# Kernel optimization log

Measured on AMD Instinct MI355X. Metric: run time of the kernel, lower is better.

Reference implementation:

```python
import jax, jax.numpy as jnp
import numpy as np

B = 4096
D_INPUT = 20
CTX = 10
IN_DIM = CTX * (D_INPUT + 1) + D_INPUT  # 230
D_MODEL = 256
N_LAYERS = 12
D_STATE = 16
D_CONV = 4
EXPAND = 2
D_INNER = EXPAND * D_MODEL  # 512
DT_RANK = (D_MODEL + 15) // 16  # ceil(256/16) = 16


def setup_inputs() -> dict:
    key = jax.random.key(0)
    ks = jax.random.split(key, 12)
    s = lambda k, shape, scale=0.02: jax.random.normal(k, shape, jnp.float32) * scale
    A = jnp.broadcast_to(jnp.arange(1, D_STATE + 1, dtype=jnp.float32), (N_LAYERS, D_INNER, D_STATE))
    return {
        "x": jax.random.normal(ks[0], (B, IN_DIM), jnp.float32),
        "Wi": s(ks[1], (IN_DIM, D_MODEL)),
        "bi": jnp.zeros((D_MODEL,), jnp.float32),
        "in_proj_w": s(ks[2], (N_LAYERS, D_MODEL, 2 * D_INNER)),
        "conv_w": s(ks[3], (N_LAYERS, D_INNER, D_CONV), 0.3),
        "conv_b": jnp.zeros((N_LAYERS, D_INNER), jnp.float32),
        "x_proj_w": s(ks[4], (N_LAYERS, D_INNER, DT_RANK + 2 * D_STATE)),
        "dt_proj_w": s(ks[5], (N_LAYERS, DT_RANK, D_INNER), 0.1),
        "dt_proj_b": jnp.full((N_LAYERS, D_INNER), -4.6, jnp.float32),  # softplus -> small dt
        "A_log": jnp.log(A),  # S4D-real init as in mamba_ssm
        "D": jnp.ones((N_LAYERS, D_INNER), jnp.float32),
        "out_proj_w": s(ks[6], (N_LAYERS, D_INNER, D_MODEL)),
        "Wo": s(ks[7], (D_MODEL, 1)),
        "bo": jnp.zeros((1,), jnp.float32),
    }


def _mamba_block(h, in_proj, conv_w, conv_b, x_proj, dt_w, dt_b, A_log, Dp, out_proj):
    # h: (B, L, D_MODEL)
    Bn, L, _ = h.shape
    xz = h @ in_proj                       # (B, L, 2*D_INNER)
    xr, z = jnp.split(xz, 2, axis=-1)
    # causal depthwise conv1d, kernel D_CONV, left-pad D_CONV-1
    xp = jnp.pad(xr, ((0, 0), (D_CONV - 1, 0), (0, 0)))
    win = jnp.stack([xp[:, k:k + L, :] for k in range(D_CONV)], axis=-1)  # (B,L,C,K)
    xc = jnp.einsum('blck,ck->blc', win, conv_w) + conv_b
    xc = jax.nn.silu(xc)
    dbl = xc @ x_proj                      # (B, L, DT_RANK + 2*D_STATE)
    dt, Bm, Cm = jnp.split(dbl, [DT_RANK, DT_RANK + D_STATE], axis=-1)
    dt = jax.nn.softplus(dt @ dt_w + dt_b)  # (B, L, D_INNER)
    A = -jnp.exp(A_log)                     # (D_INNER, D_STATE)
    dA = jnp.exp(dt[..., None] * A)                              # (B,L,di,ds)
    dBu = dt[..., None] * Bm[:, :, None, :] * xc[..., None]      # (B,L,di,ds)

    def step(hs, inp):
        dA_t, dBu_t, C_t = inp
        hs = dA_t * hs + dBu_t             # (B, di, ds)
        y_t = jnp.einsum('bds,bs->bd', hs, C_t)
        return hs, y_t

    h0 = jnp.zeros((Bn, D_INNER, D_STATE), h.dtype)
    _, ys = jax.lax.scan(step, h0, (dA.swapaxes(0, 1), dBu.swapaxes(0, 1), Cm.swapaxes(0, 1)))
    y = ys.swapaxes(0, 1)                  # (B, L, D_INNER)
    y = y + xc * Dp
    y = y * jax.nn.silu(z)
    return y @ out_proj                    # (B, L, D_MODEL)


def reference(x, Wi, bi, in_proj_w, conv_w, conv_b, x_proj_w, dt_proj_w, dt_proj_b, A_log, D, out_proj_w, Wo, bo):
    h = (x @ Wi + bi)[:, None, :]          # (B, 1, D_MODEL) -- unsqueeze(1)
    for i in range(N_LAYERS):
        h = _mamba_block(h, in_proj_w[i], conv_w[i], conv_b[i], x_proj_w[i],
                         dt_proj_w[i], dt_proj_b[i], A_log[i], D[i], out_proj_w[i])
    h = h[:, 0, :]                         # squeeze(1)
    return h @ Wo + bo                     # (B, 1)
```

## Files before the change

### kernel.cpp

```cpp
#include <hip/hip_runtime.h>
#include <hip/hip_fp8.h>
#include <math.h>

#define NB 4096
#define IN_D 230
#define DM 256
#define NL 12
#define DST 16
#define DI 512
#define DTR 16
#define XPN 48
#define XB 528
#define HB 272

typedef __attribute__((ext_vector_type(4))) float floatx4;
typedef __attribute__((ext_vector_type(2))) float floatx2;
typedef __attribute__((ext_vector_type(2))) long long2v;
typedef __attribute__((ext_vector_type(4))) int intx4;
typedef __attribute__((ext_vector_type(8))) int intx8;

__device__ __forceinline__ float silu_f(float x) {
    return x * __builtin_amdgcn_rcpf(1.0f + __expf(-x));
}
__device__ __forceinline__ float softplus_f(float x) {
    return (x > 20.0f) ? x : __logf(1.0f + __expf(x));
}

__device__ __forceinline__ unsigned char f2fp8(float x) {
#if __has_builtin(__builtin_amdgcn_cvt_pk_fp8_f32)
    return (unsigned char)(__builtin_amdgcn_cvt_pk_fp8_f32(x, x, 0, false) & 0xff);
#else
    __hip_fp8_e4m3 t(x); return (unsigned char)t.__x;
#endif
}
__device__ __forceinline__ float fp82f(unsigned char b) {
#if __has_builtin(__builtin_amdgcn_cvt_f32_fp8)
    return __builtin_amdgcn_cvt_f32_fp8((int)b, 0);
#else
    __hip_fp8_e4m3 t; t.__x = (__hip_fp8_storage_t)b; return (float)t;
#endif
}

__device__ __forceinline__ unsigned f2fp4(float x) {
    float ax = fabsf(x);
    unsigned s = (x < 0.0f) ? 8u : 0u;
    unsigned m;
    if      (ax < 0.25f) m = 0;
    else if (ax < 0.75f) m = 1;
    else if (ax < 1.25f) m = 2;
    else if (ax < 1.75f) m = 3;
    else if (ax < 2.50f) m = 4;
    else if (ax < 3.50f) m = 5;
    else if (ax < 5.00f) m = 6;
    else                 m = 7;
    return s | m;
}

__global__ __launch_bounds__(256) void pack_all(
    const float* __restrict__ x,
    const float* __restrict__ Wi, const float* __restrict__ ip,
    const float* __restrict__ op, const float* __restrict__ xp,
    const float* __restrict__ dtw,
    const float* __restrict__ cw, const float* __restrict__ cb,
    const float* __restrict__ db, const float* __restrict__ Dv,
    unsigned char* __restrict__ xpad,
    unsigned char* __restrict__ WiT, unsigned char* __restrict__ dtwP,
    unsigned char* __restrict__ ip4, unsigned char* __restrict__ op4,
    unsigned char* __restrict__ xp4,
    floatx2* __restrict__ cwcb, floatx2* __restrict__ dbdv)
{
    __shared__ float tbuf[64][65];
    const int fid = blockIdx.x;

    if (fid < 1264) {
        const float* src; unsigned char* dst;
        int K, N, ngK, t;
        bool isfp4;
        if (fid < 16) {
            src = Wi; dst = WiT; K = IN_D; N = DM; ngK = 4; t = fid; isfp4 = false;
        } else if (fid < 784) {
            int local = fid - 16; int l = local >> 6; t = local & 63;
            K = DM; N = 2 * DI; ngK = 4; isfp4 = true;
            src = ip + (size_t)l * K * N; dst = ip4 + (size_t)l * 131072;
        } else if (fid < 1168) {
            int local = fid - 784; int l = local >> 5; t = local & 31;
            K = DI; N = DM; ngK = 8; isfp4 = true;
            src = op + (size_t)l * K * N; dst = op4 + (size_t)l * 65536;
        } else {
            int local = fid - 1168; int l = local >> 3; t = local & 7;
            K = DI; N = XPN; ngK = 8; isfp4 = true;
            src = xp + (size_t)l * K * N; dst = xp4 + (size_t)l * 16384;
        }
        const int g = t % ngK, nb = t / ngK;
        const int k0 = g * 64, n0 = nb * 64;
        {
            const int r = threadIdx.x >> 6, c = threadIdx.x & 63;
#pragma unroll
            for (int i = 0; i < 16; i++) {
                int kk = k0 + i * 4 + r;
                int nn = n0 + c;
                tbuf[i * 4 + r][c] = (kk < K && nn < N) ? src[(size_t)kk * N + nn] : 0.0f;
            }
        }
        __syncthreads();
        if (!isfp4) {
            const int cbi = threadIdx.x >> 6;
            const int lane = threadIdx.x & 63;
            const int q = lane >> 4, m16 = lane & 15;
            const int chunk = (nb * 4 + cbi) * ngK + g;
            union { unsigned char b[16]; intx4 v; } buf;
#pragma unroll
            for (int sub = 0; sub < 2; sub++)
#pragma unroll
                for (int byt = 0; byt < 8; byt++) {
                    int k = sub * 32 + q * 8 + byt;
                    int n = cbi * 16 + m16;
                    buf.b[sub * 8 + byt] = f2fp8(tbuf[k][n]);
                }
            *(intx4*)(dst + (size_t)chunk * 1024 + lane * 16) = buf.v;
        } else {
            const int kg = g >> 1, half = g & 1;
            const int nkg128 = ngK >> 1;
            const int cbi = threadIdx.x >> 6;
            const int rem = threadIdx.x & 63;
            const int q4loc = rem >> 5;
            const int hb = (rem >> 4) & 1;
            const int m16 = rem & 15;
            const int q4 = half * 2 + q4loc;
            const int chunk = (nb * 4 + cbi) * nkg128 + kg;
            union { unsigned char b[8]; long v; } buf;
#pragma unroll
            for (int bl = 0; bl < 8; bl++) {
                unsigned ob = 0;
#pragma unroll
                for (int i = 0; i < 2; i++) {
                    int k_tile = q4loc * 32 + hb * 16 + bl * 2 + i;
                    float v = tbuf[k_tile][cbi * 16 + m16] * 128.0f;
                    ob |= f2fp4(v) << (i * 4);
                }
                buf.b[bl] = (unsigned char)ob;
            }
            *(long*)(dst + (size_t)chunk * 1024 + (q4 * 16 + m16) * 16 + hb * 8) = buf.v;
        }
    } else if (fid < 2032) {
        int local = fid - 1264;
        int l = local >> 6, bx = local & 63;
        int idx = bx * 256 + threadIdx.x;
        int chunk = idx >> 9;
        int rr = idx & 511;
        int lane = rr >> 3, byt = rr & 7;
        int q = lane >> 4, m16 = lane & 15;
        int col = chunk * 16 + m16;
        int k = q * 8 + byt;
        float v = (k < DTR) ? dtw[(size_t)l * DTR * DI + (size_t)k * DI + col] : 0.0f;
        dtwP[(size_t)l * 16384 + idx] = f2fp8(v);
    } else if (fid < 2056) {
        int idx = (fid - 2032) * 256 + threadIdx.x;
        floatx2 v; v.x = cw[(size_t)idx * 4 + 3]; v.y = cb[idx];
        cwcb[idx] = v;
    } else if (fid < 2080) {
        int idx = (fid - 2056) * 256 + threadIdx.x;
        floatx2 v; v.x = db[idx]; v.y = Dv[idx];
        dbdv[idx] = v;
    } else {
        int idx = (fid - 2080) * 256 + threadIdx.x;
        int r = idx >> 8, k = idx & 255;
        float v = (k < IN_D) ? x[(size_t)r * IN_D + k] : 0.0f;
        xpad[idx] = f2fp8(v);
    }
}

__global__ __launch_bounds__(1024) void mamba_all(
    const unsigned char* __restrict__ xpad, const unsigned char* __restrict__ WiT,
    const float* __restrict__ bi,
    const unsigned char* __restrict__ ip4, const unsigned char* __restrict__ op4,
    const unsigned char* __restrict__ xp4, const unsigned char* __restrict__ dtwP,
    const floatx2* __restrict__ cwcb, const floatx2* __restrict__ dbdv,
    const float* __restrict__ Wo, const float* __restrict__ bo,
    float* __restrict__ out)
{
    __shared__ unsigned char hs[16 * HB];
    __shared__ unsigned char xcs[16 * XB];
    __shared__ unsigned char szs[16 * XB];
    __shared__ float dbls[16 * 68];

    const int tid = threadIdx.x;
    const int w = tid >> 6, lane = tid & 63;
    const int q = lane >> 4, m16 = lane & 15;
    const int rb = blockIdx.x * 16;
    const long2v z2 = (long2v){0, 0};

    {
        floatx4 a0 = (floatx4){0.f, 0.f, 0.f, 0.f};
        floatx4 a1 = (floatx4){0.f, 0.f, 0.f, 0.f};
        const unsigned char* Ap = xpad + (size_t)(rb + m16) * DM + q * 8;
        const unsigned char* Bp = WiT + (size_t)(w * 4) * 1024 + lane * 16;
#pragma unroll
        for (int g = 0; g < 4; g++) {
            long2v b = *(const long2v*)(Bp + g * 1024);
            long av0 = *(const long*)(Ap + (g * 2) * 32);
            long av1 = *(const long*)(Ap + (g * 2 + 1) * 32);
            a0 = __builtin_amdgcn_mfma_f32_16x16x32_fp8_fp8(av0, b.x, a0, 0, 0, 0);
            a1 = __builtin_amdgcn_mfma_f32_16x16x32_fp8_fp8(av1, b.y, a1, 0, 0, 0);
        }
        a0 = a0 + a1;
        int col = w * 16 + m16;
#pragma unroll
        for (int r = 0; r < 4; r++)
            hs[(q * 4 + r) * HB + col] = f2fp8(a0[r] + bi[col]);
    }
    __syncthreads();

    for (int l = 0; l < NL; l++) {
        const unsigned char* ip = ip4 + (size_t)l * 131072;
        const unsigned char* xp = xp4 + (size_t)l * 16384;
        const unsigned char* op = op4 + (size_t)l * 65536;
        const unsigned char* dwp = dtwP + (size_t)l * 16384;
        const floatx2* cc = cwcb + (size_t)l * DI;
        const floatx2* dd = dbdv + (size_t)l * DI;

        {
            floatx4 acc[4];
#pragma unroll
            for (int t = 0; t < 4; t++) acc[t] = (floatx4){0.f, 0.f, 0.f, 0.f};
            const unsigned char* Bp = ip + (size_t)(w * 8) * 1024 + lane * 16;
            const unsigned char* Ar = hs + m16 * HB + q * 32;
#pragma unroll
            for (int kg = 0; kg < 2; kg++) {
                union { long2v h[2]; intx8 v; } av;
                av.h[0] = *(const long2v*)(Ar + kg * 128);
                av.h[1] = *(const long2v*)(Ar + kg * 128 + 16);
#pragma unroll
                for (int t = 0; t < 4; t++) {
                    union { long2v h[2]; intx8 v; } bv;
                    bv.h[0] = *(const long2v*)(Bp + (size_t)(t * 2 + kg) * 1024);
                    bv.h[1] = z2;
                    acc[t] = __builtin_amdgcn_mfma_scale_f32_16x16x128_f8f6f4(
                        av.v, bv.v, acc[t], 0, 4, 0, 127, 0, 120);
                }
            }
            if (w < 8) {
#pragma unroll
                for (int t = 0; t < 4; t++) {
                    int col = w * 64 + t * 16 + m16;
                    floatx2 c2 = cc[col];
#pragma unroll
                    for (int r = 0; r < 4; r++) {
                        float v = silu_f(acc[t][r] * c2.x + c2.y);
                        xcs[(q * 4 + r) * XB + col] = f2fp8(v);
                    }
                }
            } else {
#pragma unroll
                for (int t = 0; t < 4; t++)
#pragma unroll
                    for (int r = 0; r < 4; r++) {
                        int col = (w - 8) * 64 + t * 16 + m16;
                        szs[(q * 4 + r) * XB + col] = f2fp8(silu_f(acc[t][r]));
                    }
            }
        }
        __syncthreads();

        if (w < 4) {
            floatx4 acc = (floatx4){0.f, 0.f, 0.f, 0.f};
            const unsigned char* Bp = xp + (size_t)(w * 4) * 1024 + lane * 16;
            const unsigned char* Ar = xcs + m16 * XB + q * 32;
#pragma unroll
            for (int kg = 0; kg < 4; kg++) {
                union { long2v h[2]; intx8 v; } av;
                av.h[0] = *(const long2v*)(Ar + kg * 128);
                av.h[1] = *(const long2v*)(Ar + kg * 128 + 16);
                union { long2v h[2]; intx8 v; } bv;
                bv.h[0] = *(const long2v*)(Bp + (size_t)kg * 1024);
                bv.h[1] = z2;
                acc = __builtin_amdgcn_mfma_scale_f32_16x16x128_f8f6f4(
                    av.v, bv.v, acc, 0, 4, 0, 127, 0, 120);
            }
#pragma unroll
            for (int r = 0; r < 4; r++)
                dbls[(q * 4 + r) * 68 + w * 16 + m16] = acc[r];
        }
        __syncthreads();

        {
            const unsigned char* Wp = dwp + (size_t)(w * 2) * 512 + lane * 8;
            long b0 = *(const long*)(Wp);
            long b1 = *(const long*)(Wp + 512);
            const int c0 = w * 32 + m16, c1 = c0 + 16;
            const floatx2 dd0 = dd[c0], dd1 = dd[c1];

            const int brow = lane >> 2, bj = lane & 3;
            const float* dr0 = &dbls[brow * 68 + DTR];
            float p = dr0[bj]      * dr0[DST + bj]
                    + dr0[bj + 4]  * dr0[DST + bj + 4]
                    + dr0[bj + 8]  * dr0[DST + bj + 8]
                    + dr0[bj + 12] * dr0[DST + bj + 12];
            p += __shfl_xor(p, 1);
            p += __shfl_xor(p, 2);
            float bcr[4];
#pragma unroll
            for (int r = 0; r < 4; r++) bcr[r] = __shfl(p, (q * 4 + r) * 4);

            long afrag = 0;
            if (q < 2) {
                const float* dr = &dbls[m16 * 68 + q * 8];
                unsigned lo, hi;
                lo = __builtin_amdgcn_cvt_pk_fp8_f32(dr[0], dr[1], 0, false);
                lo = __builtin_amdgcn_cvt_pk_fp8_f32(dr[2], dr[3], lo, true);
                hi = __builtin_amdgcn_cvt_pk_fp8_f32(dr[4], dr[5], 0, false);
                hi = __builtin_amdgcn_cvt_pk_fp8_f32(dr[6], dr[7], hi, true);
                union { unsigned u[2]; long l; } av;
                av.u[0] = lo; av.u[1] = hi;
                afrag = av.l;
            }
            floatx4 d0v = (floatx4){dd0.x, dd0.x, dd0.x, dd0.x};
            floatx4 d1v = (floatx4){dd1.x, dd1.x, dd1.x, dd1.x};
            d0v = __builtin_amdgcn_mfma_f32_16x16x32_fp8_fp8(afrag, b0, d0v, 0, 0, 0);
            d1v = __builtin_amdgcn_mfma_f32_16x16x32_fp8_fp8(afrag, b1, d1v, 0, 0, 0);
#pragma unroll
            for (int r = 0; r < 4; r++) {
                int row = q * 4 + r;
                int off0 = row * XB + c0;
                float v0 = (softplus_f(d0v[r]) * bcr[r] + dd0.y) * fp82f(xcs[off0]) * fp82f(szs[off0]);
                xcs[off0] = f2fp8(v0);
                int off1 = off0 + 16;
                float v1 = (softplus_f(d1v[r]) * bcr[r] + dd1.y) * fp82f(xcs[off1]) * fp82f(szs[off1]);
                xcs[off1] = f2fp8(v1);
            }
        }
        __syncthreads();

        {
            floatx4 acc = (floatx4){0.f, 0.f, 0.f, 0.f};
            const unsigned char* Bp = op + (size_t)(w * 4) * 1024 + lane * 16;
            const unsigned char* Ar = xcs + m16 * XB + q * 32;
#pragma unroll
            for (int kg = 0; kg < 4; kg++) {
                union { long2v h[2]; intx8 v; } av;
                av.h[0] = *(const long2v*)(Ar + kg * 128);
                av.h[1] = *(const long2v*)(Ar + kg * 128 + 16);
                union { long2v h[2]; intx8 v; } bv;
                bv.h[0] = *(const long2v*)(Bp + (size_t)kg * 1024);
                bv.h[1] = z2;
                acc = __builtin_amdgcn_mfma_scale_f32_16x16x128_f8f6f4(
                    av.v, bv.v, acc, 0, 4, 0, 127, 0, 120);
            }
            int col = w * 16 + m16;
#pragma unroll
            for (int r = 0; r < 4; r++)
                hs[(q * 4 + r) * HB + col] = f2fp8(acc[r]);
        }
        __syncthreads();
    }

    {
        float s = 0.0f;
#pragma unroll
        for (int j = 0; j < 4; j++)
            s += fp82f(hs[w * HB + lane * 4 + j]) * Wo[lane * 4 + j];
#pragma unroll
        for (int off = 32; off > 0; off >>= 1) s += __shfl_down(s, off);
        if (lane == 0) out[rb + w] = s + bo[0];
    }
}

extern "C" void kernel_launch(void* const* d_in, const int* in_sizes, int n_in,
                              void* d_out, int out_size, void* d_ws, size_t ws_size,
                              hipStream_t stream)
{
    const float* x       = (const float*)d_in[0];
    const float* Wi      = (const float*)d_in[1];
    const float* bi      = (const float*)d_in[2];
    const float* in_proj = (const float*)d_in[3];
    const float* conv_w  = (const float*)d_in[4];
    const float* conv_b  = (const float*)d_in[5];
    const float* x_proj  = (const float*)d_in[6];
    const float* dt_w    = (const float*)d_in[7];
    const float* dt_b    = (const float*)d_in[8];
    const float* Dp      = (const float*)d_in[10];
    const float* out_pw  = (const float*)d_in[11];
    const float* Wo      = (const float*)d_in[12];
    const float* bo      = (const float*)d_in[13];

    unsigned char* ws = (unsigned char*)d_ws;
    unsigned char* xpad = ws;
    unsigned char* WiT  = xpad + (size_t)NB * DM;
    unsigned char* dtwP = WiT + (size_t)DM * DM;
    floatx2* cwcb = (floatx2*)(dtwP + (size_t)NL * 16384);
    floatx2* dbdv = cwcb + (size_t)NL * DI;
    unsigned char* ip4 = (unsigned char*)(dbdv + (size_t)NL * DI);
    unsigned char* op4 = ip4 + (size_t)NL * 131072;
    unsigned char* xp4 = op4 + (size_t)NL * 65536;

    pack_all<<<dim3(6176), dim3(256), 0, stream>>>(
        x, Wi, in_proj, out_pw, x_proj, dt_w, conv_w, conv_b, dt_b, Dp,
        xpad, WiT, dtwP, ip4, op4, xp4, cwcb, dbdv);

    mamba_all<<<dim3(NB / 16), dim3(1024), 0, stream>>>(
        xpad, WiT, bi, ip4, op4, xp4, dtwP,
        cwcb, dbdv, Wo, bo, (float*)d_out);
}
```

Before: 176.8 us.

## Prefetch next layer's weights into registers with double-buffered layer loop

Weight fragments for the in_proj, dt_proj and out_proj matmuls of the next layer are loaded into registers while the current layer computes, using two register sets that alternate across a two-layer unrolled loop. This hides global/L2 load latency behind the layer's barriers and compute. It raises register pressure (launch bounds now request 4 blocks per CU-ish occupancy hint) and performs one redundant prefetch of layer 0 at the end.

```diff
diff --git a/kernel.cpp b/kernel.cpp
--- a/kernel.cpp
+++ b/kernel.cpp
@@ -170,7 +170,170 @@
     }
 }
 
-__global__ __launch_bounds__(1024) void mamba_all(
+
+#define PRELOAD(LL, S1, B0, B1, S4) do {                                          \
+    const int ln_ = (LL);                                                         \
+    const unsigned char* bp1_ = ip4 + (size_t)ln_ * 131072                        \
+                              + (size_t)(w * 8) * 1024 + (size_t)lane * 16;       \
+    S1[0] = *(const long2v*)(bp1_);                                               \
+    S1[1] = *(const long2v*)(bp1_ + 1024);                                        \
+    S1[2] = *(const long2v*)(bp1_ + 2048);                                        \
+    S1[3] = *(const long2v*)(bp1_ + 3072);                                        \
+    S1[4] = *(const long2v*)(bp1_ + 4096);                                        \
+    S1[5] = *(const long2v*)(bp1_ + 5120);                                        \
+    S1[6] = *(const long2v*)(bp1_ + 6144);                                        \
+    S1[7] = *(const long2v*)(bp1_ + 7168);                                        \
+    const unsigned char* wp_ = dtwP + (size_t)ln_ * 16384                         \
+                             + (size_t)(w * 2) * 512 + (size_t)lane * 8;          \
+    B0 = *(const long*)(wp_);                                                     \
+    B1 = *(const long*)(wp_ + 512);                                               \
+    const unsigned char* bp4_ = op4 + (size_t)ln_ * 65536                         \
+                              + (size_t)(w * 4) * 1024 + (size_t)lane * 16;       \
+    S4[0] = *(const long2v*)(bp4_);                                               \
+    S4[1] = *(const long2v*)(bp4_ + 1024);                                        \
+    S4[2] = *(const long2v*)(bp4_ + 2048);                                        \
+    S4[3] = *(const long2v*)(bp4_ + 3072);                                        \
+} while (0)
+
+#define LAYER(LCUR, S1, B0, B1, S4, LNXT, S1N, B0N, B1N, S4N) do {                \
+    const int l_ = (LCUR);                                                        \
+    const unsigned char* xp = xp4 + (size_t)l_ * 16384;                           \
+    const floatx2* cc = cwcb + (size_t)l_ * DI;                                   \
+    const floatx2* dd = dbdv + (size_t)l_ * DI;                                   \
+    \
+    {                                                                             \
+        floatx4 acc[4];                                                           \
+        _Pragma("unroll")                                                         \
+        for (int t = 0; t < 4; t++) acc[t] = (floatx4){0.f, 0.f, 0.f, 0.f};       \
+        const unsigned char* Ar = hs + m16 * HB + q * 32;                         \
+        _Pragma("unroll")                                                         \
+        for (int kg = 0; kg < 2; kg++) {                                          \
+            union { long2v h[2]; intx8 v; } av;                                   \
+            av.h[0] = *(const long2v*)(Ar + kg * 128);                            \
+            av.h[1] = *(const long2v*)(Ar + kg * 128 + 16);                       \
+            _Pragma("unroll")                                                     \
+            for (int t = 0; t < 4; t++) {                                         \
+                union { long2v h[2]; intx8 v; } bv;                               \
+                bv.h[0] = S1[t * 2 + kg];                                         \
+                bv.h[1] = z2;                                                     \
+                acc[t] = __builtin_amdgcn_mfma_scale_f32_16x16x128_f8f6f4(        \
+                    av.v, bv.v, acc[t], 0, 4, 0, 127, 0, 120);                    \
+            }                                                                     \
+        }                                                                         \
+              \
+        PRELOAD(LNXT, S1N, B0N, B1N, S4N);                                        \
+        if (w < 8) {                                                              \
+            _Pragma("unroll")                                                     \
+            for (int t = 0; t < 4; t++) {                                         \
+                int col = w * 64 + t * 16 + m16;                                  \
+                floatx2 c2 = cc[col];                                             \
+                _Pragma("unroll")                                                 \
+                for (int r = 0; r < 4; r++) {                                     \
+                    float v = silu_f(acc[t][r] * c2.x + c2.y);                    \
+                    xcs[(q * 4 + r) * XB + col] = f2fp8(v);                       \
+                }                                                                 \
+            }                                                                     \
+        } else {                                                                  \
+            _Pragma("unroll")                                                     \
+            for (int t = 0; t < 4; t++)                                           \
+                _Pragma("unroll")                                                 \
+                for (int r = 0; r < 4; r++) {                                     \
+                    int col = (w - 8) * 64 + t * 16 + m16;                        \
+                    szs[(q * 4 + r) * XB + col] = f2fp8(silu_f(acc[t][r]));       \
+                }                                                                 \
+        }                                                                         \
+    }                                                                             \
+    __syncthreads();                                                              \
+           \
+    if (w < 4) {                                                                  \
+        floatx4 acc = (floatx4){0.f, 0.f, 0.f, 0.f};                              \
+        const unsigned char* Bp = xp + (size_t)(w * 4) * 1024 + lane * 16;        \
+        const unsigned char* Ar = xcs + m16 * XB + q * 32;                        \
+        _Pragma("unroll")                                                         \
+        for (int kg = 0; kg < 4; kg++) {                                          \
+            union { long2v h[2]; intx8 v; } av;                                   \
+            av.h[0] = *(const long2v*)(Ar + kg * 128);                            \
+            av.h[1] = *(const long2v*)(Ar + kg * 128 + 16);                       \
+            union { long2v h[2]; intx8 v; } bv;                                   \
+            bv.h[0] = *(const long2v*)(Bp + (size_t)kg * 1024);                   \
+            bv.h[1] = z2;                                                         \
+            acc = __builtin_amdgcn_mfma_scale_f32_16x16x128_f8f6f4(               \
+                av.v, bv.v, acc, 0, 4, 0, 127, 0, 120);                           \
+        }                                                                         \
+        _Pragma("unroll")                                                         \
+        for (int r = 0; r < 4; r++)                                               \
+            dbls[(q * 4 + r) * 68 + w * 16 + m16] = acc[r];                       \
+    }                                                                             \
+    __syncthreads();                                                              \
+       \
+    {                                                                             \
+        const int c0 = w * 32 + m16, c1 = c0 + 16;                                \
+        const floatx2 dd0 = dd[c0], dd1 = dd[c1];                                 \
+        const int brow = lane >> 2, bj = lane & 3;                                \
+        const float* dr0 = &dbls[brow * 68 + DTR];                                \
+        float p = dr0[bj]      * dr0[DST + bj]                                    \
+                + dr0[bj + 4]  * dr0[DST + bj + 4]                                \
+                + dr0[bj + 8]  * dr0[DST + bj + 8]                                \
+                + dr0[bj + 12] * dr0[DST + bj + 12];                              \
+        p += __shfl_xor(p, 1);                                                    \
+        p += __shfl_xor(p, 2);                                                    \
+        float bcr[4];                                                             \
+        _Pragma("unroll")                                                         \
+        for (int r = 0; r < 4; r++) bcr[r] = __shfl(p, (q * 4 + r) * 4);          \
+        long afrag = 0;                                                           \
+        if (q < 2) {                                                              \
+            const float* dr = &dbls[m16 * 68 + q * 8];                            \
+            unsigned lo, hi;                                                      \
+            lo = __builtin_amdgcn_cvt_pk_fp8_f32(dr[0], dr[1], 0, false);         \
+            lo = __builtin_amdgcn_cvt_pk_fp8_f32(dr[2], dr[3], lo, true);         \
+            hi = __builtin_amdgcn_cvt_pk_fp8_f32(dr[4], dr[5], 0, false);         \
+            hi = __builtin_amdgcn_cvt_pk_fp8_f32(dr[6], dr[7], hi, true);         \
+            union { unsigned u[2]; long l; } av;                                  \
+            av.u[0] = lo; av.u[1] = hi;                                           \
+            afrag = av.l;                                                         \
+        }                                                                         \
+        floatx4 d0v = (floatx4){dd0.x, dd0.x, dd0.x, dd0.x};                      \
+        floatx4 d1v = (floatx4){dd1.x, dd1.x, dd1.x, dd1.x};                      \
+        d0v = __builtin_amdgcn_mfma_f32_16x16x32_fp8_fp8(afrag, B0, d0v, 0, 0, 0);\
+        d1v = __builtin_amdgcn_mfma_f32_16x16x32_fp8_fp8(afrag, B1, d1v, 0, 0, 0);\
+        _Pragma("unroll")                                                         \
+        for (int r = 0; r < 4; r++) {                                             \
+            int row = q * 4 + r;                                                  \
+            int off0 = row * XB + c0;                                             \
+            float v0 = (softplus_f(d0v[r]) * bcr[r] + dd0.y)                      \
+                     * fp82f(xcs[off0]) * fp82f(szs[off0]);                       \
+            xcs[off0] = f2fp8(v0);                                                \
+            int off1 = off0 + 16;                                                 \
+            float v1 = (softplus_f(d1v[r]) * bcr[r] + dd1.y)                      \
+                     * fp82f(xcs[off1]) * fp82f(szs[off1]);                       \
+            xcs[off1] = f2fp8(v1);                                                \
+        }                                                                         \
+    }                                                                             \
+    __syncthreads();                                                              \
+                \
+    {                                                                             \
+        floatx4 acc = (floatx4){0.f, 0.f, 0.f, 0.f};                              \
+        const unsigned char* Ar = xcs + m16 * XB + q * 32;                        \
+        _Pragma("unroll")                                                         \
+        for (int kg = 0; kg < 4; kg++) {                                          \
+            union { long2v h[2]; intx8 v; } av;                                   \
+            av.h[0] = *(const long2v*)(Ar + kg * 128);                            \
+            av.h[1] = *(const long2v*)(Ar + kg * 128 + 16);                       \
+            union { long2v h[2]; intx8 v; } bv;                                   \
+            bv.h[0] = S4[kg];                                                     \
+            bv.h[1] = z2;                                                         \
+            acc = __builtin_amdgcn_mfma_scale_f32_16x16x128_f8f6f4(               \
+                av.v, bv.v, acc, 0, 4, 0, 127, 0, 120);                           \
+        }                                                                         \
+        int col = w * 16 + m16;                                                   \
+        _Pragma("unroll")                                                         \
+        for (int r = 0; r < 4; r++)                                               \
+            hs[(q * 4 + r) * HB + col] = f2fp8(acc[r]);                           \
+    }                                                                             \
+    __syncthreads();                                                              \
+} while (0)
+
+__global__ __launch_bounds__(1024, 4) void mamba_all(
     const unsigned char* __restrict__ xpad, const unsigned char* __restrict__ WiT,
     const float* __restrict__ bi,
     const unsigned char* __restrict__ ip4, const unsigned char* __restrict__ op4,
@@ -190,6 +353,9 @@
     const int rb = blockIdx.x * 16;
     const long2v z2 = (long2v){0, 0};
 
+    long2v s1a[8], s1b[8], s4a[4], s4b[4];
+    long b0a, b1a, b0b, b1b;
+
     {
         floatx4 a0 = (floatx4){0.f, 0.f, 0.f, 0.f};
         floatx4 a1 = (floatx4){0.f, 0.f, 0.f, 0.f};
@@ -203,6 +369,7 @@
             a0 = __builtin_amdgcn_mfma_f32_16x16x32_fp8_fp8(av0, b.x, a0, 0, 0, 0);
             a1 = __builtin_amdgcn_mfma_f32_16x16x32_fp8_fp8(av1, b.y, a1, 0, 0, 0);
         }
+        PRELOAD(0, s1a, b0a, b1a, s4a);
         a0 = a0 + a1;
         int col = w * 16 + m16;
 #pragma unroll
@@ -211,147 +378,9 @@
     }
     __syncthreads();
 
-    for (int l = 0; l < NL; l++) {
-        const unsigned char* ip = ip4 + (size_t)l * 131072;
-        const unsigned char* xp = xp4 + (size_t)l * 16384;
-        const unsigned char* op = op4 + (size_t)l * 65536;
-        const unsigned char* dwp = dtwP + (size_t)l * 16384;
-        const floatx2* cc = cwcb + (size_t)l * DI;
-        const floatx2* dd = dbdv + (size_t)l * DI;
-
-        {
-            floatx4 acc[4];
-#pragma unroll
-            for (int t = 0; t < 4; t++) acc[t] = (floatx4){0.f, 0.f, 0.f, 0.f};
-            const unsigned char* Bp = ip + (size_t)(w * 8) * 1024 + lane * 16;
-            const unsigned char* Ar = hs + m16 * HB + q * 32;
-#pragma unroll
-            for (int kg = 0; kg < 2; kg++) {
-                union { long2v h[2]; intx8 v; } av;
-                av.h[0] = *(const long2v*)(Ar + kg * 128);
-                av.h[1] = *(const long2v*)(Ar + kg * 128 + 16);
-#pragma unroll
-                for (int t = 0; t < 4; t++) {
-                    union { long2v h[2]; intx8 v; } bv;
-                    bv.h[0] = *(const long2v*)(Bp + (size_t)(t * 2 + kg) * 1024);
-                    bv.h[1] = z2;
-                    acc[t] = __builtin_amdgcn_mfma_scale_f32_16x16x128_f8f6f4(
-                        av.v, bv.v, acc[t], 0, 4, 0, 127, 0, 120);
-                }
-            }
-            if (w < 8) {
-#pragma unroll
-                for (int t = 0; t < 4; t++) {
-                    int col = w * 64 + t * 16 + m16;
-                    floatx2 c2 = cc[col];
-#pragma unroll
-                    for (int r = 0; r < 4; r++) {
-                        float v = silu_f(acc[t][r] * c2.x + c2.y);
-                        xcs[(q * 4 + r) * XB + col] = f2fp8(v);
-                    }
-                }
-            } else {
-#pragma unroll
-                for (int t = 0; t < 4; t++)
-#pragma unroll
-                    for (int r = 0; r < 4; r++) {
-                        int col = (w - 8) * 64 + t * 16 + m16;
-                        szs[(q * 4 + r) * XB + col] = f2fp8(silu_f(acc[t][r]));
-                    }
-            }
-        }
-        __syncthreads();
-
-        if (w < 4) {
-            floatx4 acc = (floatx4){0.f, 0.f, 0.f, 0.f};
-            const unsigned char* Bp = xp + (size_t)(w * 4) * 1024 + lane * 16;
-            const unsigned char* Ar = xcs + m16 * XB + q * 32;
-#pragma unroll
-            for (int kg = 0; kg < 4; kg++) {
-                union { long2v h[2]; intx8 v; } av;
-                av.h[0] = *(const long2v*)(Ar + kg * 128);
-                av.h[1] = *(const long2v*)(Ar + kg * 128 + 16);
-                union { long2v h[2]; intx8 v; } bv;
-                bv.h[0] = *(const long2v*)(Bp + (size_t)kg * 1024);
-                bv.h[1] = z2;
-                acc = __builtin_amdgcn_mfma_scale_f32_16x16x128_f8f6f4(
-                    av.v, bv.v, acc, 0, 4, 0, 127, 0, 120);
-            }
-#pragma unroll
-            for (int r = 0; r < 4; r++)
-                dbls[(q * 4 + r) * 68 + w * 16 + m16] = acc[r];
-        }
-        __syncthreads();
-
-        {
-            const unsigned char* Wp = dwp + (size_t)(w * 2) * 512 + lane * 8;
-            long b0 = *(const long*)(Wp);
-            long b1 = *(const long*)(Wp + 512);
-            const int c0 = w * 32 + m16, c1 = c0 + 16;
-            const floatx2 dd0 = dd[c0], dd1 = dd[c1];
-
-            const int brow = lane >> 2, bj = lane & 3;
-            const float* dr0 = &dbls[brow * 68 + DTR];
-            float p = dr0[bj]      * dr0[DST + bj]
-                    + dr0[bj + 4]  * dr0[DST + bj + 4]
-                    + dr0[bj + 8]  * dr0[DST + bj + 8]
-                    + dr0[bj + 12] * dr0[DST + bj + 12];
-            p += __shfl_xor(p, 1);
-            p += __shfl_xor(p, 2);
-            float bcr[4];
-#pragma unroll
-            for (int r = 0; r < 4; r++) bcr[r] = __shfl(p, (q * 4 + r) * 4);
-
-            long afrag = 0;
-            if (q < 2) {
-                const float* dr = &dbls[m16 * 68 + q * 8];
-                unsigned lo, hi;
-                lo = __builtin_amdgcn_cvt_pk_fp8_f32(dr[0], dr[1], 0, false);
-                lo = __builtin_amdgcn_cvt_pk_fp8_f32(dr[2], dr[3], lo, true);
-                hi = __builtin_amdgcn_cvt_pk_fp8_f32(dr[4], dr[5], 0, false);
-                hi = __builtin_amdgcn_cvt_pk_fp8_f32(dr[6], dr[7], hi, true);
-                union { unsigned u[2]; long l; } av;
-                av.u[0] = lo; av.u[1] = hi;
-                afrag = av.l;
-            }
-            floatx4 d0v = (floatx4){dd0.x, dd0.x, dd0.x, dd0.x};
-            floatx4 d1v = (floatx4){dd1.x, dd1.x, dd1.x, dd1.x};
-            d0v = __builtin_amdgcn_mfma_f32_16x16x32_fp8_fp8(afrag, b0, d0v, 0, 0, 0);
-            d1v = __builtin_amdgcn_mfma_f32_16x16x32_fp8_fp8(afrag, b1, d1v, 0, 0, 0);
-#pragma unroll
-            for (int r = 0; r < 4; r++) {
-                int row = q * 4 + r;
-                int off0 = row * XB + c0;
-                float v0 = (softplus_f(d0v[r]) * bcr[r] + dd0.y) * fp82f(xcs[off0]) * fp82f(szs[off0]);
-                xcs[off0] = f2fp8(v0);
-                int off1 = off0 + 16;
-                float v1 = (softplus_f(d1v[r]) * bcr[r] + dd1.y) * fp82f(xcs[off1]) * fp82f(szs[off1]);
-                xcs[off1] = f2fp8(v1);
-            }
-        }
-        __syncthreads();
-
-        {
-            floatx4 acc = (floatx4){0.f, 0.f, 0.f, 0.f};
-            const unsigned char* Bp = op + (size_t)(w * 4) * 1024 + lane * 16;
-            const unsigned char* Ar = xcs + m16 * XB + q * 32;
-#pragma unroll
-            for (int kg = 0; kg < 4; kg++) {
-                union { long2v h[2]; intx8 v; } av;
-                av.h[0] = *(const long2v*)(Ar + kg * 128);
-                av.h[1] = *(const long2v*)(Ar + kg * 128 + 16);
-                union { long2v h[2]; intx8 v; } bv;
-                bv.h[0] = *(const long2v*)(Bp + (size_t)kg * 1024);
-                bv.h[1] = z2;
-                acc = __builtin_amdgcn_mfma_scale_f32_16x16x128_f8f6f4(
-                    av.v, bv.v, acc, 0, 4, 0, 127, 0, 120);
-            }
-            int col = w * 16 + m16;
-#pragma unroll
-            for (int r = 0; r < 4; r++)
-                hs[(q * 4 + r) * HB + col] = f2fp8(acc[r]);
-        }
-        __syncthreads();
+    for (int l = 0; l < NL; l += 2) {
+        LAYER(l,     s1a, b0a, b1a, s4a, l + 1,                     s1b, b0b, b1b, s4b);
+        LAYER(l + 1, s1b, b0b, b1b, s4b, (l + 2 < NL) ? l + 2 : 0,  s1a, b0a, b1a, s4a);
     }
 
     {
```

Result: slower. 265.7 us (+50.3%).

## Swap MFMA operand roles to get packed 4-byte fp8 stores to shared memory

Applied to the files above, without the earlier changes.

The MFMA operands are swapped so weights become the A operand and activations the B operand. Each lane then holds four consecutive columns of one row and can write them as a single packed 32-bit fp8 word instead of four strided byte stores. The pack kernel is also vectorised to convert four values per thread, which cuts its grid size, and the final reduction uses packed loads. The change reduces LDS byte stores and conversion instructions, but it depends on the swapped scale and format arguments staying numerically equivalent.

```diff
diff --git a/kernel.cpp b/kernel.cpp
--- a/kernel.cpp
+++ b/kernel.cpp
@@ -39,6 +39,14 @@
 #else
     __hip_fp8_e4m3 t; t.__x = (__hip_fp8_storage_t)b; return (float)t;
 #endif
+}
+__device__ __forceinline__ unsigned pk4fp8(float a, float b, float c, float d) {
+    unsigned w = __builtin_amdgcn_cvt_pk_fp8_f32(a, b, 0, false);
+    return __builtin_amdgcn_cvt_pk_fp8_f32(c, d, w, true);
+}
+template<int S>
+__device__ __forceinline__ float fp8sel(unsigned w) {
+    return __builtin_amdgcn_cvt_f32_fp8((int)w, S);
 }
 
 __device__ __forceinline__ unsigned f2fp4(float x) {
@@ -142,31 +150,41 @@
             }
             *(long*)(dst + (size_t)chunk * 1024 + (q4 * 16 + m16) * 16 + hb * 8) = buf.v;
         }
-    } else if (fid < 2032) {
-        int local = fid - 1264;
-        int l = local >> 6, bx = local & 63;
-        int idx = bx * 256 + threadIdx.x;
-        int chunk = idx >> 9;
-        int rr = idx & 511;
-        int lane = rr >> 3, byt = rr & 7;
+    } else if (fid < 1456) {
+        int gid = (fid - 1264) * 256 + threadIdx.x;
+        int idx = gid * 4;
+        int l = idx >> 14;
+        int r14 = idx & 16383;
+        int chunk = r14 >> 9;
+        int rr = r14 & 511;
+        int lane = rr >> 3, byt0 = rr & 7;
         int q = lane >> 4, m16 = lane & 15;
         int col = chunk * 16 + m16;
-        int k = q * 8 + byt;
-        float v = (k < DTR) ? dtw[(size_t)l * DTR * DI + (size_t)k * DI + col] : 0.0f;
-        dtwP[(size_t)l * 16384 + idx] = f2fp8(v);
-    } else if (fid < 2056) {
-        int idx = (fid - 2032) * 256 + threadIdx.x;
+        float v[4];
+#pragma unroll
+        for (int j = 0; j < 4; j++) {
+            int k = q * 8 + byt0 + j;
+            v[j] = (k < DTR) ? dtw[(size_t)l * DTR * DI + (size_t)k * DI + col] : 0.0f;
+        }
+        *(unsigned*)(dtwP + idx) = pk4fp8(v[0], v[1], v[2], v[3]);
+    } else if (fid < 1480) {
+        int idx = (fid - 1456) * 256 + threadIdx.x;
         floatx2 v; v.x = cw[(size_t)idx * 4 + 3]; v.y = cb[idx];
         cwcb[idx] = v;
-    } else if (fid < 2080) {
-        int idx = (fid - 2056) * 256 + threadIdx.x;
+    } else if (fid < 1504) {
+        int idx = (fid - 1480) * 256 + threadIdx.x;
         floatx2 v; v.x = db[idx]; v.y = Dv[idx];
         dbdv[idx] = v;
     } else {
-        int idx = (fid - 2080) * 256 + threadIdx.x;
-        int r = idx >> 8, k = idx & 255;
-        float v = (k < IN_D) ? x[(size_t)r * IN_D + k] : 0.0f;
-        xpad[idx] = f2fp8(v);
+        int gid = (fid - 1504) * 256 + threadIdx.x;
+        int r = gid >> 6, c4 = (gid & 63) * 4;
+        float v[4];
+#pragma unroll
+        for (int j = 0; j < 4; j++) {
+            int k = c4 + j;
+            v[j] = (k < IN_D) ? x[(size_t)r * IN_D + k] : 0.0f;
+        }
+        *(unsigned*)(xpad + (size_t)gid * 4) = pk4fp8(v[0], v[1], v[2], v[3]);
     }
 }
 
@@ -193,28 +211,27 @@
     {
         floatx4 a0 = (floatx4){0.f, 0.f, 0.f, 0.f};
         floatx4 a1 = (floatx4){0.f, 0.f, 0.f, 0.f};
-        const unsigned char* Ap = xpad + (size_t)(rb + m16) * DM + q * 8;
-        const unsigned char* Bp = WiT + (size_t)(w * 4) * 1024 + lane * 16;
+        const unsigned char* Bp = xpad + (size_t)(rb + m16) * DM + q * 8;
+        const unsigned char* Ap = WiT + (size_t)(w * 4) * 1024 + lane * 16;
 #pragma unroll
         for (int g = 0; g < 4; g++) {
-            long2v b = *(const long2v*)(Bp + g * 1024);
-            long av0 = *(const long*)(Ap + (g * 2) * 32);
-            long av1 = *(const long*)(Ap + (g * 2 + 1) * 32);
-            a0 = __builtin_amdgcn_mfma_f32_16x16x32_fp8_fp8(av0, b.x, a0, 0, 0, 0);
-            a1 = __builtin_amdgcn_mfma_f32_16x16x32_fp8_fp8(av1, b.y, a1, 0, 0, 0);
+            long2v a = *(const long2v*)(Ap + g * 1024);
+            long bv0 = *(const long*)(Bp + (g * 2) * 32);
+            long bv1 = *(const long*)(Bp + (g * 2 + 1) * 32);
+            a0 = __builtin_amdgcn_mfma_f32_16x16x32_fp8_fp8(a.x, bv0, a0, 0, 0, 0);
+            a1 = __builtin_amdgcn_mfma_f32_16x16x32_fp8_fp8(a.y, bv1, a1, 0, 0, 0);
         }
         a0 = a0 + a1;
-        int col = w * 16 + m16;
-#pragma unroll
-        for (int r = 0; r < 4; r++)
-            hs[(q * 4 + r) * HB + col] = f2fp8(a0[r] + bi[col]);
+        floatx4 b4 = *(const floatx4*)(bi + w * 16 + q * 4);
+        *(unsigned*)(hs + m16 * HB + w * 16 + q * 4) =
+            pk4fp8(a0[0] + b4[0], a0[1] + b4[1], a0[2] + b4[2], a0[3] + b4[3]);
     }
     __syncthreads();
 
     for (int l = 0; l < NL; l++) {
-        const unsigned char* ip = ip4 + (size_t)l * 131072;
-        const unsigned char* xp = xp4 + (size_t)l * 16384;
-        const unsigned char* op = op4 + (size_t)l * 65536;
+        const unsigned char* ipw = ip4 + (size_t)l * 131072;
+        const unsigned char* xpw = xp4 + (size_t)l * 16384;
+        const unsigned char* opw = op4 + (size_t)l * 65536;
         const unsigned char* dwp = dtwP + (size_t)l * 16384;
         const floatx2* cc = cwcb + (size_t)l * DI;
         const floatx2* dd = dbdv + (size_t)l * DI;
@@ -223,72 +240,70 @@
             floatx4 acc[4];
 #pragma unroll
             for (int t = 0; t < 4; t++) acc[t] = (floatx4){0.f, 0.f, 0.f, 0.f};
-            const unsigned char* Bp = ip + (size_t)(w * 8) * 1024 + lane * 16;
-            const unsigned char* Ar = hs + m16 * HB + q * 32;
+            const unsigned char* Ap = ipw + (size_t)(w * 8) * 1024 + lane * 16;
+            const unsigned char* Br = hs + m16 * HB + q * 32;
 #pragma unroll
             for (int kg = 0; kg < 2; kg++) {
-                union { long2v h[2]; intx8 v; } av;
-                av.h[0] = *(const long2v*)(Ar + kg * 128);
-                av.h[1] = *(const long2v*)(Ar + kg * 128 + 16);
+                union { long2v h[2]; intx8 v; } bv;
+                bv.h[0] = *(const long2v*)(Br + kg * 128);
+                bv.h[1] = *(const long2v*)(Br + kg * 128 + 16);
 #pragma unroll
                 for (int t = 0; t < 4; t++) {
-                    union { long2v h[2]; intx8 v; } bv;
-                    bv.h[0] = *(const long2v*)(Bp + (size_t)(t * 2 + kg) * 1024);
-                    bv.h[1] = z2;
+                    union { long2v h[2]; intx8 v; } av;
+                    av.h[0] = *(const long2v*)(Ap + (size_t)(t * 2 + kg) * 1024);
+                    av.h[1] = z2;
                     acc[t] = __builtin_amdgcn_mfma_scale_f32_16x16x128_f8f6f4(
-                        av.v, bv.v, acc[t], 0, 4, 0, 127, 0, 120);
+                        av.v, bv.v, acc[t], 4, 0, 0, 120, 0, 127);
                 }
             }
             if (w < 8) {
 #pragma unroll
                 for (int t = 0; t < 4; t++) {
-                    int col = w * 64 + t * 16 + m16;
-                    floatx2 c2 = cc[col];
-#pragma unroll
-                    for (int r = 0; r < 4; r++) {
-                        float v = silu_f(acc[t][r] * c2.x + c2.y);
-                        xcs[(q * 4 + r) * XB + col] = f2fp8(v);
-                    }
+                    int colb = w * 64 + t * 16 + q * 4;
+                    floatx4 cA = *(const floatx4*)(cc + colb);
+                    floatx4 cB = *(const floatx4*)(cc + colb + 2);
+                    float v0 = silu_f(acc[t][0] * cA[0] + cA[1]);
+                    float v1 = silu_f(acc[t][1] * cA[2] + cA[3]);
+                    float v2 = silu_f(acc[t][2] * cB[0] + cB[1]);
+                    float v3 = silu_f(acc[t][3] * cB[2] + cB[3]);
+                    *(unsigned*)(xcs + m16 * XB + colb) = pk4fp8(v0, v1, v2, v3);
                 }
             } else {
 #pragma unroll
-                for (int t = 0; t < 4; t++)
-#pragma unroll
-                    for (int r = 0; r < 4; r++) {
-                        int col = (w - 8) * 64 + t * 16 + m16;
-                        szs[(q * 4 + r) * XB + col] = f2fp8(silu_f(acc[t][r]));
-                    }
+                for (int t = 0; t < 4; t++) {
+                    int colb = (w - 8) * 64 + t * 16 + q * 4;
+                    *(unsigned*)(szs + m16 * XB + colb) =
+                        pk4fp8(silu_f(acc[t][0]), silu_f(acc[t][1]),
+                               silu_f(acc[t][2]), silu_f(acc[t][3]));
+                }
             }
         }
         __syncthreads();
 
         if (w < 4) {
             floatx4 acc = (floatx4){0.f, 0.f, 0.f, 0.f};
-            const unsigned char* Bp = xp + (size_t)(w * 4) * 1024 + lane * 16;
-            const unsigned char* Ar = xcs + m16 * XB + q * 32;
+            const unsigned char* Ap = xpw + (size_t)(w * 4) * 1024 + lane * 16;
+            const unsigned char* Br = xcs + m16 * XB + q * 32;
 #pragma unroll
             for (int kg = 0; kg < 4; kg++) {
+                union { long2v h[2]; intx8 v; } bv;
+                bv.h[0] = *(const long2v*)(Br + kg * 128);
+                bv.h[1] = *(const long2v*)(Br + kg * 128 + 16);
                 union { long2v h[2]; intx8 v; } av;
-                av.h[0] = *(const long2v*)(Ar + kg * 128);
-                av.h[1] = *(const long2v*)(Ar + kg * 128 + 16);
-                union { long2v h[2]; intx8 v; } bv;
-                bv.h[0] = *(const long2v*)(Bp + (size_t)kg * 1024);
-                bv.h[1] = z2;
+                av.h[0] = *(const long2v*)(Ap + (size_t)kg * 1024);
+                av.h[1] = z2;
                 acc = __builtin_amdgcn_mfma_scale_f32_16x16x128_f8f6f4(
-                    av.v, bv.v, acc, 0, 4, 0, 127, 0, 120);
-            }
-#pragma unroll
-            for (int r = 0; r < 4; r++)
-                dbls[(q * 4 + r) * 68 + w * 16 + m16] = acc[r];
+                    av.v, bv.v, acc, 4, 0, 0, 120, 0, 127);
+            }
+            *(floatx4*)(&dbls[m16 * 68 + w * 16 + q * 4]) = acc;
         }
         __syncthreads();
 
         {
             const unsigned char* Wp = dwp + (size_t)(w * 2) * 512 + lane * 8;
-            long b0 = *(const long*)(Wp);
-            long b1 = *(const long*)(Wp + 512);
-            const int c0 = w * 32 + m16, c1 = c0 + 16;
-            const floatx2 dd0 = dd[c0], dd1 = dd[c1];
+            long a0 = *(const long*)(Wp);
+            long a1 = *(const long*)(Wp + 512);
+            const int cb0 = w * 32 + q * 4;
 
             const int brow = lane >> 2, bj = lane & 3;
             const float* dr0 = &dbls[brow * 68 + DTR];
@@ -298,67 +313,73 @@
                     + dr0[bj + 12] * dr0[DST + bj + 12];
             p += __shfl_xor(p, 1);
             p += __shfl_xor(p, 2);
-            float bcr[4];
-#pragma unroll
-            for (int r = 0; r < 4; r++) bcr[r] = __shfl(p, (q * 4 + r) * 4);
-
-            long afrag = 0;
+            float bcv = __shfl(p, m16 * 4);
+
+            long bfrag = 0;
             if (q < 2) {
                 const float* dr = &dbls[m16 * 68 + q * 8];
-                unsigned lo, hi;
-                lo = __builtin_amdgcn_cvt_pk_fp8_f32(dr[0], dr[1], 0, false);
-                lo = __builtin_amdgcn_cvt_pk_fp8_f32(dr[2], dr[3], lo, true);
-                hi = __builtin_amdgcn_cvt_pk_fp8_f32(dr[4], dr[5], 0, false);
-                hi = __builtin_amdgcn_cvt_pk_fp8_f32(dr[6], dr[7], hi, true);
-                union { unsigned u[2]; long l; } av;
-                av.u[0] = lo; av.u[1] = hi;
-                afrag = av.l;
-            }
-            floatx4 d0v = (floatx4){dd0.x, dd0.x, dd0.x, dd0.x};
-            floatx4 d1v = (floatx4){dd1.x, dd1.x, dd1.x, dd1.x};
-            d0v = __builtin_amdgcn_mfma_f32_16x16x32_fp8_fp8(afrag, b0, d0v, 0, 0, 0);
-            d1v = __builtin_amdgcn_mfma_f32_16x16x32_fp8_fp8(afrag, b1, d1v, 0, 0, 0);
-#pragma unroll
-            for (int r = 0; r < 4; r++) {
-                int row = q * 4 + r;
-                int off0 = row * XB + c0;
-                float v0 = (softplus_f(d0v[r]) * bcr[r] + dd0.y) * fp82f(xcs[off0]) * fp82f(szs[off0]);
-                xcs[off0] = f2fp8(v0);
-                int off1 = off0 + 16;
-                float v1 = (softplus_f(d1v[r]) * bcr[r] + dd1.y) * fp82f(xcs[off1]) * fp82f(szs[off1]);
-                xcs[off1] = f2fp8(v1);
-            }
+                union { unsigned u[2]; long l; } uv;
+                uv.u[0] = pk4fp8(dr[0], dr[1], dr[2], dr[3]);
+                uv.u[1] = pk4fp8(dr[4], dr[5], dr[6], dr[7]);
+                bfrag = uv.l;
+            }
+
+            floatx4 dA = *(const floatx4*)(dd + cb0);
+            floatx4 dB = *(const floatx4*)(dd + cb0 + 2);
+            floatx4 dC = *(const floatx4*)(dd + cb0 + 16);
+            floatx4 dD = *(const floatx4*)(dd + cb0 + 18);
+            floatx4 d0v = (floatx4){dA[0], dA[2], dB[0], dB[2]};
+            floatx4 d1v = (floatx4){dC[0], dC[2], dD[0], dD[2]};
+            floatx4 Dv0 = (floatx4){dA[1], dA[3], dB[1], dB[3]};
+            floatx4 Dv1 = (floatx4){dC[1], dC[3], dD[1], dD[3]};
+            d0v = __builtin_amdgcn_mfma_f32_16x16x32_fp8_fp8(a0, bfrag, d0v, 0, 0, 0);
+            d1v = __builtin_amdgcn_mfma_f32_16x16x32_fp8_fp8(a1, bfrag, d1v, 0, 0, 0);
+
+            const int off = m16 * XB + cb0;
+            unsigned xw0 = *(const unsigned*)(xcs + off);
+            unsigned zw0 = *(const unsigned*)(szs + off);
+            unsigned xw1 = *(const unsigned*)(xcs + off + 16);
+            unsigned zw1 = *(const unsigned*)(szs + off + 16);
+            float y0[4], y1[4];
+            y0[0] = (softplus_f(d0v[0]) * bcv + Dv0[0]) * fp8sel<0>(xw0) * fp8sel<0>(zw0);
+            y0[1] = (softplus_f(d0v[1]) * bcv + Dv0[1]) * fp8sel<1>(xw0) * fp8sel<1>(zw0);
+            y0[2] = (softplus_f(d0v[2]) * bcv + Dv0[2]) * fp8sel<2>(xw0) * fp8sel<2>(zw0);
+            y0[3] = (softplus_f(d0v[3]) * bcv + Dv0[3]) * fp8sel<3>(xw0) * fp8sel<3>(zw0);
+            y1[0] = (softplus_f(d1v[0]) * bcv + Dv1[0]) * fp8sel<0>(xw1) * fp8sel<0>(zw1);
+            y1[1] = (softplus_f(d1v[1]) * bcv + Dv1[1]) * fp8sel<1>(xw1) * fp8sel<1>(zw1);
+            y1[2] = (softplus_f(d1v[2]) * bcv + Dv1[2]) * fp8sel<2>(xw1) * fp8sel<2>(zw1);
+            y1[3] = (softplus_f(d1v[3]) * bcv + Dv1[3]) * fp8sel<3>(xw1) * fp8sel<3>(zw1);
+            *(unsigned*)(xcs + off)      = pk4fp8(y0[0], y0[1], y0[2], y0[3]);
+            *(unsigned*)(xcs + off + 16) = pk4fp8(y1[0], y1[1], y1[2], y1[3]);
         }
         __syncthreads();
 
         {
             floatx4 acc = (floatx4){0.f, 0.f, 0.f, 0.f};
-            const unsigned char* Bp = op + (size_t)(w * 4) * 1024 + lane * 16;
-            const unsigned char* Ar = xcs + m16 * XB + q * 32;
+            const unsigned char* Ap = opw + (size_t)(w * 4) * 1024 + lane * 16;
+            const unsigned char* Br = xcs + m16 * XB + q * 32;
 #pragma unroll
             for (int kg = 0; kg < 4; kg++) {
+                union { long2v h[2]; intx8 v; } bv;
+                bv.h[0] = *(const long2v*)(Br + kg * 128);
+                bv.h[1] = *(const long2v*)(Br + kg * 128 + 16);
                 union { long2v h[2]; intx8 v; } av;
-                av.h[0] = *(const long2v*)(Ar + kg * 128);
-                av.h[1] = *(const long2v*)(Ar + kg * 128 + 16);
-                union { long2v h[2]; intx8 v; } bv;
-                bv.h[0] = *(const long2v*)(Bp + (size_t)kg * 1024);
-                bv.h[1] = z2;
+                av.h[0] = *(const long2v*)(Ap + (size_t)kg * 1024);
+                av.h[1] = z2;
                 acc = __builtin_amdgcn_mfma_scale_f32_16x16x128_f8f6f4(
-                    av.v, bv.v, acc, 0, 4, 0, 127, 0, 120);
-            }
-            int col = w * 16 + m16;
-#pragma unroll
-            for (int r = 0; r < 4; r++)
-                hs[(q * 4 + r) * HB + col] = f2fp8(acc[r]);
+                    av.v, bv.v, acc, 4, 0, 0, 120, 0, 127);
+            }
+            *(unsigned*)(hs + m16 * HB + w * 16 + q * 4) =
+                pk4fp8(acc[0], acc[1], acc[2], acc[3]);
         }
         __syncthreads();
     }
 
     {
-        float s = 0.0f;
-#pragma unroll
-        for (int j = 0; j < 4; j++)
-            s += fp82f(hs[w * HB + lane * 4 + j]) * Wo[lane * 4 + j];
+        unsigned hw = *(const unsigned*)(hs + w * HB + lane * 4);
+        floatx4 w4 = *(const floatx4*)(Wo + lane * 4);
+        float s = fp8sel<0>(hw) * w4[0] + fp8sel<1>(hw) * w4[1]
+                + fp8sel<2>(hw) * w4[2] + fp8sel<3>(hw) * w4[3];
 #pragma unroll
         for (int off = 32; off > 0; off >>= 1) s += __shfl_down(s, off);
         if (lane == 0) out[rb + w] = s + bo[0];
@@ -393,7 +414,7 @@
     unsigned char* op4 = ip4 + (size_t)NL * 131072;
     unsigned char* xp4 = op4 + (size_t)NL * 65536;
 
-    pack_all<<<dim3(6176), dim3(256), 0, stream>>>(
+    pack_all<<<dim3(2528), dim3(256), 0, stream>>>(
         x, Wi, in_proj, out_pw, x_proj, dt_w, conv_w, conv_b, dt_b, Dp,
         xpad, WiT, dtwP, ip4, op4, xp4, cwcb, dbdv);
 
```

Result: slower. 180.7 us (+2.2%).
